# Performance work log

Measured on AMD Instinct MI355X. Metric: run time of the kernel, lower is better.

The kernel has to match this reference:

```python
import jax, jax.numpy as jnp
import numpy as np

B, S, IN, OUT = 64, 512, 256, 256   # batch, seq_len, in/out features
R, NB, E = 40, 3, 262144            # num_rels, num_bases, num_edges
N = B * S                           # total nodes in batched graph


def setup_inputs() -> dict:
    key = jax.random.key(0)
    ks = jax.random.split(key, 6)
    text = jax.random.normal(ks[0], (B, S, IN), jnp.float32)
    src = jax.random.randint(ks[1], (E,), 0, N)
    dst = jax.random.randint(ks[2], (E,), 0, N)
    rel = jax.random.randint(ks[3], (E,), 0, R)
    bases = jax.random.normal(ks[4], (NB, IN, OUT), jnp.float32) / np.sqrt(IN).astype(np.float32)
    comp = jax.random.normal(ks[5], (R, NB), jnp.float32)
    bias = jnp.zeros((OUT,), jnp.float32)
    return dict(text=text, src=src, dst=dst, rel=rel, bases=bases, comp=comp, bias=bias)


def reference(text, src, dst, rel, bases, comp, bias):
    Bt, St, INt = text.shape
    h = text.reshape(-1, INt)                       # [N, in] flattened node feats
    n_nodes = h.shape[0]
    # project every node through every basis once: [N, num_bases, out]
    t = jnp.einsum('ni,bio->nbo', h, bases)
    # per-edge message: sum_b comp[rel_e, b] * (h_src @ basis_b)  -> [E, out]
    msg = jnp.einsum('eb,ebo->eo', comp[rel], t[src])
    # scatter-sum aggregation to destination nodes
    agg = jax.ops.segment_sum(msg, dst, num_segments=n_nodes)   # [N, out]
    out = jax.nn.relu(agg + bias)
    return out.reshape(Bt, -1, out.shape[-1])
```

## Files before the change

kernel.cpp:

```cpp
#include <hip/hip_runtime.h>
#include <cstdint>

#define N_NODES 32768
#define IN_F    256
#define OUT_F   256
#define NBASES  3
#define N_EDGES 262144
#define K_DIM   (NBASES * IN_F)

typedef __attribute__((ext_vector_type(8))) short bf16x8;
typedef __attribute__((ext_vector_type(4))) float f32x4;

__device__ __forceinline__ unsigned short f2bf(float x) {
    union { float f; unsigned int u; } c; c.f = x;
    unsigned int u = c.u;
    u = (u + 0x7FFFu + ((u >> 16) & 1u)) >> 16;
    return (unsigned short)u;
}
__device__ __forceinline__ float bf2f(unsigned short h) {
    union { unsigned int u; float f; } c; c.u = ((unsigned int)h) << 16;
    return c.f;
}

__device__ __forceinline__ void async_copy16(const void* g, void* l) {
    __builtin_amdgcn_global_load_lds(
        (const __attribute__((address_space(1))) unsigned int*)g,
        (__attribute__((address_space(3))) unsigned int*)l, 16, 0, 0);
}

__global__ __launch_bounds__(256) void prep_kernel(
    const float* __restrict__ text,
    const float* __restrict__ bases,
    unsigned short* __restrict__ hb,
    unsigned short* __restrict__ Wt,
    int* __restrict__ counts)
{
    const int tid = threadIdx.x;
    if (blockIdx.x < 8192) {
        if (!hb) return;
        int i = blockIdx.x * 256 + tid;
        float4 v = reinterpret_cast<const float4*>(text)[i];
        ushort4 o;
        o.x = f2bf(v.x); o.y = f2bf(v.y); o.z = f2bf(v.z); o.w = f2bf(v.w);
        reinterpret_cast<ushort4*>(hb)[i] = o;
    } else if (blockIdx.x < 8384) {
        int tb = blockIdx.x - 8192;
        int kb = tb % 24, ob = tb / 24;
        __shared__ float tile[32][33];
        int c = tid & 31, r8 = tid >> 5;
        #pragma unroll
        for (int i = 0; i < 4; ++i) {
            int r = r8 + 8 * i;
            tile[r][c] = bases[(size_t)(kb * 32 + r) * OUT_F + ob * 32 + c];
        }
        __syncthreads();
        #pragma unroll
        for (int i = 0; i < 4; ++i) {
            int r = r8 + 8 * i;
            Wt[(size_t)(ob * 32 + r) * K_DIM + kb * 32 + c] = f2bf(tile[c][r]);
        }
    } else {
        int i = (blockIdx.x - 8384) * 256 + tid;
        counts[i] = 0;
    }
}

__global__ __launch_bounds__(256) void hist_kernel(
    const int* __restrict__ dst, int* __restrict__ counts)
{
    int e4 = blockIdx.x * 256 + threadIdx.x;
    int4 d = reinterpret_cast<const int4*>(dst)[e4];
    atomicAdd(&counts[d.x], 1);
    atomicAdd(&counts[d.y], 1);
    atomicAdd(&counts[d.z], 1);
    atomicAdd(&counts[d.w], 1);
}

__global__ __launch_bounds__(1024) void scan_kernel(
    int* __restrict__ counts,
    int* __restrict__ offsets)
{
    __shared__ int wsum[16];
    const int tid = threadIdx.x;
    const int wave = tid >> 6, lane = tid & 63;
    const int base = tid * 32;
    int local[32];
    int sum = 0;
    #pragma unroll
    for (int k8 = 0; k8 < 8; ++k8) {
        int4 v = reinterpret_cast<const int4*>(counts + base)[k8];
        local[k8 * 4 + 0] = v.x; local[k8 * 4 + 1] = v.y;
        local[k8 * 4 + 2] = v.z; local[k8 * 4 + 3] = v.w;
        sum += v.x + v.y + v.z + v.w;
    }
    int inc = sum;
    #pragma unroll
    for (int off = 1; off < 64; off <<= 1) {
        int v = __shfl_up(inc, off);
        if (lane >= off) inc += v;
    }
    if (lane == 63) wsum[wave] = inc;
    __syncthreads();
    if (wave == 0 && lane < 16) {
        int v = wsum[lane];
        #pragma unroll
        for (int off = 1; off < 16; off <<= 1) {
            int u = __shfl_up(v, off);
            if (lane >= off) v += u;
        }
        wsum[lane] = v;
    }
    __syncthreads();
    int run = inc - sum + (wave ? wsum[wave - 1] : 0);
    #pragma unroll
    for (int k = 0; k < 32; ++k) {
        offsets[base + k] = run;
        counts[base + k] = run;
        run += local[k];
    }
    if (tid == 1023) offsets[N_NODES] = run;
}

__global__ __launch_bounds__(256) void scatter_kernel(
    const int* __restrict__ dst, const int* __restrict__ src,
    const int* __restrict__ rel, int* __restrict__ cursor,
    int* __restrict__ packed)
{
    int e4 = blockIdx.x * 256 + threadIdx.x;
    int4 d = reinterpret_cast<const int4*>(dst)[e4];
    int4 s = reinterpret_cast<const int4*>(src)[e4];
    int4 r = reinterpret_cast<const int4*>(rel)[e4];
    int p0 = atomicAdd(&cursor[d.x], 1);
    packed[p0] = (r.x << 16) | s.x;
    int p1 = atomicAdd(&cursor[d.y], 1);
    packed[p1] = (r.y << 16) | s.y;
    int p2 = atomicAdd(&cursor[d.z], 1);
    packed[p2] = (r.z << 16) | s.z;
    int p3 = atomicAdd(&cursor[d.w], 1);
    packed[p3] = (r.w << 16) | s.w;
}

__global__ __launch_bounds__(256) void agg_bf16_kernel(
    const unsigned short* __restrict__ hb,
    const int* __restrict__ packed,
    const int* __restrict__ offsets,
    const float* __restrict__ comp,
    unsigned short* __restrict__ z)
{
    __shared__ float compS[128];
    if (threadIdx.x < 120) compS[threadIdx.x] = comp[threadIdx.x];
    __syncthreads();

    const int node = blockIdx.x * 4 + (threadIdx.x >> 6);
    const int lane = threadIdx.x & 63;
    const int start = offsets[node];
    const int end   = offsets[node + 1];

    float a0[4] = {}, a1[4] = {}, a2[4] = {};

    for (int cb = start; cb < end; cb += 64) {
        int idx = cb + lane;
        int pv = (idx < end) ? packed[idx] : 0;
        int cnt = min(64, end - cb);
        for (int j = 0; j < cnt; j += 4) {
            float c0[4], c1[4], c2[4];
            ushort4 u[4];
            #pragma unroll
            for (int q = 0; q < 4; ++q) {
                int p = __shfl(pv, j + q);
                int s = p & 0xFFFF, r = p >> 16;
                float m = (j + q < cnt) ? 1.f : 0.f;
                c0[q] = m * compS[r * 3 + 0];
                c1[q] = m * compS[r * 3 + 1];
                c2[q] = m * compS[r * 3 + 2];
                u[q] = *reinterpret_cast<const ushort4*>(
                    hb + (size_t)s * IN_F + lane * 4);
            }
            #pragma unroll
            for (int q = 0; q < 4; ++q) {
                float v[4] = { bf2f(u[q].x), bf2f(u[q].y),
                               bf2f(u[q].z), bf2f(u[q].w) };
                #pragma unroll
                for (int k = 0; k < 4; ++k) {
                    a0[k] += c0[q] * v[k];
                    a1[k] += c1[q] * v[k];
                    a2[k] += c2[q] * v[k];
                }
            }
        }
    }

    unsigned short* zp = z + (size_t)node * K_DIM + lane * 4;
    ushort4 o;
    o.x = f2bf(a0[0]); o.y = f2bf(a0[1]); o.z = f2bf(a0[2]); o.w = f2bf(a0[3]);
    *reinterpret_cast<ushort4*>(zp) = o;
    o.x = f2bf(a1[0]); o.y = f2bf(a1[1]); o.z = f2bf(a1[2]); o.w = f2bf(a1[3]);
    *reinterpret_cast<ushort4*>(zp + 256) = o;
    o.x = f2bf(a2[0]); o.y = f2bf(a2[1]); o.z = f2bf(a2[2]); o.w = f2bf(a2[3]);
    *reinterpret_cast<ushort4*>(zp + 512) = o;
}

__global__ __launch_bounds__(256) void agg_f32_kernel(
    const float* __restrict__ h,
    const int* __restrict__ packed,
    const int* __restrict__ offsets,
    const float* __restrict__ comp,
    unsigned short* __restrict__ z)
{
    __shared__ float compS[128];
    if (threadIdx.x < 120) compS[threadIdx.x] = comp[threadIdx.x];
    __syncthreads();
    const int node = blockIdx.x * 4 + (threadIdx.x >> 6);
    const int lane = threadIdx.x & 63;
    const int start = offsets[node];
    const int end   = offsets[node + 1];
    float a0[4] = {}, a1[4] = {}, a2[4] = {};
    for (int cb = start; cb < end; cb += 64) {
        int idx = cb + lane;
        int pv = (idx < end) ? packed[idx] : 0;
        int cnt = min(64, end - cb);
        for (int j = 0; j < cnt; ++j) {
            int p = __shfl(pv, j);
            int s = p & 0xFFFF, r = p >> 16;
            float c0 = compS[r*3], c1 = compS[r*3+1], c2 = compS[r*3+2];
            float4 v = *reinterpret_cast<const float4*>(
                h + (size_t)s * IN_F + lane * 4);
            a0[0] += c0*v.x; a0[1] += c0*v.y; a0[2] += c0*v.z; a0[3] += c0*v.w;
            a1[0] += c1*v.x; a1[1] += c1*v.y; a1[2] += c1*v.z; a1[3] += c1*v.w;
            a2[0] += c2*v.x; a2[1] += c2*v.y; a2[2] += c2*v.z; a2[3] += c2*v.w;
        }
    }
    unsigned short* zp = z + (size_t)node * K_DIM + lane * 4;
    ushort4 o;
    o.x = f2bf(a0[0]); o.y = f2bf(a0[1]); o.z = f2bf(a0[2]); o.w = f2bf(a0[3]);
    *reinterpret_cast<ushort4*>(zp) = o;
    o.x = f2bf(a1[0]); o.y = f2bf(a1[1]); o.z = f2bf(a1[2]); o.w = f2bf(a1[3]);
    *reinterpret_cast<ushort4*>(zp + 256) = o;
    o.x = f2bf(a2[0]); o.y = f2bf(a2[1]); o.z = f2bf(a2[2]); o.w = f2bf(a2[3]);
    *reinterpret_cast<ushort4*>(zp + 512) = o;
}

__global__ __launch_bounds__(256) void gemm_kernel(
    const unsigned short* __restrict__ A,
    const unsigned short* __restrict__ Bt,
    const float* __restrict__ bias,
    float* __restrict__ out)
{
    __shared__ __align__(16) unsigned short As[2][64 * 32];
    __shared__ __align__(16) unsigned short Bs[2][128 * 32];

    const int tid  = threadIdx.x;
    const int wave = tid >> 6, lane = tid & 63;
    const int quad = lane >> 4, l16 = lane & 15;
    const int wm = (wave & 1) * 32, wn = (wave >> 1) * 64;
    const int m0 = blockIdx.x * 64, n0 = blockIdx.y * 128;

    f32x4 acc[2][4] = {};

    const int pa   = wave * 64 + lane;
    const int rowa = pa >> 2;
    const int octa = (pa & 3) ^ ((rowa >> 1) & 3);
    const unsigned short* ga = A + (size_t)(m0 + rowa) * K_DIM + octa * 8;
    const int la_off = (wave * 64) * 8;

    const unsigned short* gb[2];
    int lb_off[2];
    #pragma unroll
    for (int c = 0; c < 2; ++c) {
        int p   = c * 256 + wave * 64 + lane;
        int row = p >> 2;
        int oct = (p & 3) ^ ((row >> 1) & 3);
        gb[c] = Bt + (size_t)(n0 + row) * K_DIM + oct * 8;
        lb_off[c] = (c * 256 + wave * 64) * 8;
    }

    async_copy16(ga, &As[0][la_off]);
    async_copy16(gb[0], &Bs[0][lb_off[0]]);
    async_copy16(gb[1], &Bs[0][lb_off[1]]);

    int cur = 0;
    for (int step = 0; step < K_DIM / 32; ++step) {
        __syncthreads();
        int k1 = (step + 1) * 32;
        if (k1 < K_DIM) {
            async_copy16(ga + k1, &As[cur ^ 1][la_off]);
            async_copy16(gb[0] + k1, &Bs[cur ^ 1][lb_off[0]]);
            async_copy16(gb[1] + k1, &Bs[cur ^ 1][lb_off[1]]);
        }

        bf16x8 af[2], bfr[4];
        #pragma unroll
        for (int i = 0; i < 2; ++i) {
            int row = wm + i * 16 + l16;
            int oph = quad ^ ((row >> 1) & 3);
            af[i] = *reinterpret_cast<const bf16x8*>(&As[cur][(row * 4 + oph) * 8]);
        }
        #pragma unroll
        for (int j = 0; j < 4; ++j) {
            int nn   = wn + j * 16 + l16;
            int oph2 = quad ^ ((nn >> 1) & 3);
            bfr[j] = *reinterpret_cast<const bf16x8*>(&Bs[cur][(nn * 4 + oph2) * 8]);
        }
        #pragma unroll
        for (int i = 0; i < 2; ++i)
            #pragma unroll
            for (int j = 0; j < 4; ++j)
                acc[i][j] = __builtin_amdgcn_mfma_f32_16x16x32_bf16(
                    af[i], bfr[j], acc[i][j], 0, 0, 0);
        cur ^= 1;
    }

    #pragma unroll
    for (int j = 0; j < 4; ++j) {
        int col = n0 + wn + j * 16 + l16;
        float bv = bias[col];
        #pragma unroll
        for (int i = 0; i < 2; ++i) {
            int row_base = m0 + wm + i * 16 + quad * 4;
            #pragma unroll
            for (int r = 0; r < 4; ++r)
                out[(size_t)(row_base + r) * OUT_F + col] =
                    fmaxf(acc[i][j][r] + bv, 0.f);
        }
    }
}

extern "C" void kernel_launch(void* const* d_in, const int* in_sizes, int n_in,
                              void* d_out, int out_size, void* d_ws, size_t ws_size,
                              hipStream_t stream) {
    const float* text  = (const float*)d_in[0];
    const int*   src   = (const int*)d_in[1];
    const int*   dst   = (const int*)d_in[2];
    const int*   rel   = (const int*)d_in[3];
    const float* bases = (const float*)d_in[4];
    const float* comp  = (const float*)d_in[5];
    const float* bias  = (const float*)d_in[6];
    float* out = (float*)d_out;

    char* p = (char*)d_ws;
    unsigned short* z = (unsigned short*)p;       p += (size_t)N_NODES * K_DIM * 2;
    int* packed  = (int*)p;                       p += (size_t)N_EDGES * 4;
    int* offsets = (int*)p;                       p += (size_t)(N_NODES + 4) * 4;
    int* counts  = (int*)p;                       p += (size_t)N_NODES * 4;
    unsigned short* Wt = (unsigned short*)p;      p += (size_t)OUT_F * K_DIM * 2;
    bool use_bf16_h = (ws_size >= (size_t)(p - (char*)d_ws) + (size_t)N_NODES * IN_F * 2);
    unsigned short* hb = use_bf16_h ? (unsigned short*)p : nullptr;

    prep_kernel<<<8512, 256, 0, stream>>>(text, bases, hb, Wt, counts);
    hist_kernel<<<N_EDGES / 1024, 256, 0, stream>>>(dst, counts);
    scan_kernel<<<1, 1024, 0, stream>>>(counts, offsets);
    scatter_kernel<<<N_EDGES / 1024, 256, 0, stream>>>(dst, src, rel, counts, packed);
    if (use_bf16_h)
        agg_bf16_kernel<<<N_NODES / 4, 256, 0, stream>>>(hb, packed, offsets, comp, z);
    else
        agg_f32_kernel<<<N_NODES / 4, 256, 0, stream>>>(text, packed, offsets, comp, z);
    gemm_kernel<<<dim3(N_NODES / 64, OUT_F / 128), 256, 0, stream>>>(
        z, Wt, bias, out);
}
```

Measured before the change: 193.4 us.

## Fuse edge aggregation with basis GEMM and pack bf16 coefficients into edge records

Merges the per-node aggregation kernel and the GEMM into one kernel. Each block aggregates 32 destination nodes into a swizzled LDS tile and then runs MFMA against the transposed basis weights, so the intermediate z matrix (N x 768 bf16) is never written to or read back from global memory. The scatter kernel now precomputes the three relation coefficients as bf16 and stores them alongside the source index in an 8-byte record, which removes the comp lookup from the gather loop but rounds the coefficients to bf16. The GEMM loses double-buffered B loads and the full Wt is streamed once per 32-row block. The f32 fallback path is dropped and the code assumes the workspace is large enough.

```diff
diff --git a/kernel.cpp b/kernel.cpp
--- a/kernel.cpp
+++ b/kernel.cpp
@@ -7,6 +7,7 @@
 #define NBASES  3
 #define N_EDGES 262144
 #define K_DIM   (NBASES * IN_F)
+#define ZROWS   32
 
 typedef __attribute__((ext_vector_type(8))) short bf16x8;
 typedef __attribute__((ext_vector_type(4))) float f32x4;
@@ -37,7 +38,6 @@
 {
     const int tid = threadIdx.x;
     if (blockIdx.x < 8192) {
-        if (!hb) return;
         int i = blockIdx.x * 256 + tid;
         float4 v = reinterpret_cast<const float4*>(text)[i];
         ushort4 o;
@@ -123,183 +123,128 @@
 
 __global__ __launch_bounds__(256) void scatter_kernel(
     const int* __restrict__ dst, const int* __restrict__ src,
-    const int* __restrict__ rel, int* __restrict__ cursor,
-    int* __restrict__ packed)
+    const int* __restrict__ rel, const float* __restrict__ comp,
+    int* __restrict__ cursor, int2* __restrict__ packed2)
 {
     int e4 = blockIdx.x * 256 + threadIdx.x;
     int4 d = reinterpret_cast<const int4*>(dst)[e4];
     int4 s = reinterpret_cast<const int4*>(src)[e4];
     int4 r = reinterpret_cast<const int4*>(rel)[e4];
-    int p0 = atomicAdd(&cursor[d.x], 1);
-    packed[p0] = (r.x << 16) | s.x;
-    int p1 = atomicAdd(&cursor[d.y], 1);
-    packed[p1] = (r.y << 16) | s.y;
-    int p2 = atomicAdd(&cursor[d.z], 1);
-    packed[p2] = (r.z << 16) | s.z;
-    int p3 = atomicAdd(&cursor[d.w], 1);
-    packed[p3] = (r.w << 16) | s.w;
-}
-
-__global__ __launch_bounds__(256) void agg_bf16_kernel(
+    int dd[4] = { d.x, d.y, d.z, d.w };
+    int ss[4] = { s.x, s.y, s.z, s.w };
+    int rr[4] = { r.x, r.y, r.z, r.w };
+    #pragma unroll
+    for (int q = 0; q < 4; ++q) {
+        float c0 = comp[rr[q] * 3 + 0];
+        float c1 = comp[rr[q] * 3 + 1];
+        float c2 = comp[rr[q] * 3 + 2];
+        int w0 = ss[q] | ((int)f2bf(c0) << 16);
+        int w1 = (int)f2bf(c1) | ((int)f2bf(c2) << 16);
+        int pos = atomicAdd(&cursor[dd[q]], 1);
+        packed2[pos] = make_int2(w0, w1);
+    }
+}
+
+__global__ __launch_bounds__(256, 2) void fused_kernel(
     const unsigned short* __restrict__ hb,
-    const int* __restrict__ packed,
+    const int2* __restrict__ packed2,
     const int* __restrict__ offsets,
-    const float* __restrict__ comp,
-    unsigned short* __restrict__ z)
-{
-    __shared__ float compS[128];
-    if (threadIdx.x < 120) compS[threadIdx.x] = comp[threadIdx.x];
-    __syncthreads();
-
-    const int node = blockIdx.x * 4 + (threadIdx.x >> 6);
-    const int lane = threadIdx.x & 63;
-    const int start = offsets[node];
-    const int end   = offsets[node + 1];
-
-    float a0[4] = {}, a1[4] = {}, a2[4] = {};
-
-    for (int cb = start; cb < end; cb += 64) {
-        int idx = cb + lane;
-        int pv = (idx < end) ? packed[idx] : 0;
-        int cnt = min(64, end - cb);
-        for (int j = 0; j < cnt; j += 4) {
-            float c0[4], c1[4], c2[4];
-            ushort4 u[4];
-            #pragma unroll
-            for (int q = 0; q < 4; ++q) {
-                int p = __shfl(pv, j + q);
-                int s = p & 0xFFFF, r = p >> 16;
-                float m = (j + q < cnt) ? 1.f : 0.f;
-                c0[q] = m * compS[r * 3 + 0];
-                c1[q] = m * compS[r * 3 + 1];
-                c2[q] = m * compS[r * 3 + 2];
-                u[q] = *reinterpret_cast<const ushort4*>(
-                    hb + (size_t)s * IN_F + lane * 4);
-            }
-            #pragma unroll
-            for (int q = 0; q < 4; ++q) {
-                float v[4] = { bf2f(u[q].x), bf2f(u[q].y),
-                               bf2f(u[q].z), bf2f(u[q].w) };
-                #pragma unroll
-                for (int k = 0; k < 4; ++k) {
-                    a0[k] += c0[q] * v[k];
-                    a1[k] += c1[q] * v[k];
-                    a2[k] += c2[q] * v[k];
-                }
-            }
-        }
-    }
-
-    unsigned short* zp = z + (size_t)node * K_DIM + lane * 4;
-    ushort4 o;
-    o.x = f2bf(a0[0]); o.y = f2bf(a0[1]); o.z = f2bf(a0[2]); o.w = f2bf(a0[3]);
-    *reinterpret_cast<ushort4*>(zp) = o;
-    o.x = f2bf(a1[0]); o.y = f2bf(a1[1]); o.z = f2bf(a1[2]); o.w = f2bf(a1[3]);
-    *reinterpret_cast<ushort4*>(zp + 256) = o;
-    o.x = f2bf(a2[0]); o.y = f2bf(a2[1]); o.z = f2bf(a2[2]); o.w = f2bf(a2[3]);
-    *reinterpret_cast<ushort4*>(zp + 512) = o;
-}
-
-__global__ __launch_bounds__(256) void agg_f32_kernel(
-    const float* __restrict__ h,
-    const int* __restrict__ packed,
-    const int* __restrict__ offsets,
-    const float* __restrict__ comp,
-    unsigned short* __restrict__ z)
-{
-    __shared__ float compS[128];
-    if (threadIdx.x < 120) compS[threadIdx.x] = comp[threadIdx.x];
-    __syncthreads();
-    const int node = blockIdx.x * 4 + (threadIdx.x >> 6);
-    const int lane = threadIdx.x & 63;
-    const int start = offsets[node];
-    const int end   = offsets[node + 1];
-    float a0[4] = {}, a1[4] = {}, a2[4] = {};
-    for (int cb = start; cb < end; cb += 64) {
-        int idx = cb + lane;
-        int pv = (idx < end) ? packed[idx] : 0;
-        int cnt = min(64, end - cb);
-        for (int j = 0; j < cnt; ++j) {
-            int p = __shfl(pv, j);
-            int s = p & 0xFFFF, r = p >> 16;
-            float c0 = compS[r*3], c1 = compS[r*3+1], c2 = compS[r*3+2];
-            float4 v = *reinterpret_cast<const float4*>(
-                h + (size_t)s * IN_F + lane * 4);
-            a0[0] += c0*v.x; a0[1] += c0*v.y; a0[2] += c0*v.z; a0[3] += c0*v.w;
-            a1[0] += c1*v.x; a1[1] += c1*v.y; a1[2] += c1*v.z; a1[3] += c1*v.w;
-            a2[0] += c2*v.x; a2[1] += c2*v.y; a2[2] += c2*v.z; a2[3] += c2*v.w;
-        }
-    }
-    unsigned short* zp = z + (size_t)node * K_DIM + lane * 4;
-    ushort4 o;
-    o.x = f2bf(a0[0]); o.y = f2bf(a0[1]); o.z = f2bf(a0[2]); o.w = f2bf(a0[3]);
-    *reinterpret_cast<ushort4*>(zp) = o;
-    o.x = f2bf(a1[0]); o.y = f2bf(a1[1]); o.z = f2bf(a1[2]); o.w = f2bf(a1[3]);
-    *reinterpret_cast<ushort4*>(zp + 256) = o;
-    o.x = f2bf(a2[0]); o.y = f2bf(a2[1]); o.z = f2bf(a2[2]); o.w = f2bf(a2[3]);
-    *reinterpret_cast<ushort4*>(zp + 512) = o;
-}
-
-__global__ __launch_bounds__(256) void gemm_kernel(
-    const unsigned short* __restrict__ A,
-    const unsigned short* __restrict__ Bt,
+    const unsigned short* __restrict__ Wt,
     const float* __restrict__ bias,
     float* __restrict__ out)
 {
-    __shared__ __align__(16) unsigned short As[2][64 * 32];
-    __shared__ __align__(16) unsigned short Bs[2][128 * 32];
+    __shared__ __align__(16) unsigned short Zs[ZROWS * 96 * 8];
+    __shared__ __align__(16) unsigned short Bs[256 * 4 * 8];
 
     const int tid  = threadIdx.x;
     const int wave = tid >> 6, lane = tid & 63;
     const int quad = lane >> 4, l16 = lane & 15;
-    const int wm = (wave & 1) * 32, wn = (wave >> 1) * 64;
-    const int m0 = blockIdx.x * 64, n0 = blockIdx.y * 128;
+    const int m0 = blockIdx.x * ZROWS;
+
+    for (int i = 0; i < 8; ++i) {
+        const int m = wave * 8 + i;
+        const int node = m0 + m;
+        const int start = offsets[node];
+        const int end   = offsets[node + 1];
+
+        float a[12] = {};
+        for (int cb = start; cb < end; cb += 64) {
+            int idx = cb + lane;
+            int wx = 0, wy = 0;
+            if (idx < end) { int2 w = packed2[idx]; wx = w.x; wy = w.y; }
+            int cnt = min(64, end - cb);
+            for (int j = 0; j < cnt; j += 4) {
+                float c0[4], c1[4], c2[4];
+                ushort4 u[4];
+                #pragma unroll
+                for (int q = 0; q < 4; ++q) {
+                    int p0 = __shfl(wx, j + q);
+                    int p1 = __shfl(wy, j + q);
+                    int s = p0 & 0xFFFF;
+                    c0[q] = bf2f((unsigned short)((unsigned)p0 >> 16));
+                    c1[q] = bf2f((unsigned short)(p1 & 0xFFFF));
+                    c2[q] = bf2f((unsigned short)((unsigned)p1 >> 16));
+                    u[q] = *reinterpret_cast<const ushort4*>(
+                        hb + (size_t)s * IN_F + lane * 4);
+                }
+                #pragma unroll
+                for (int q = 0; q < 4; ++q) {
+                    float v[4] = { bf2f(u[q].x), bf2f(u[q].y),
+                                   bf2f(u[q].z), bf2f(u[q].w) };
+                    #pragma unroll
+                    for (int k = 0; k < 4; ++k) {
+                        a[k]     += c0[q] * v[k];
+                        a[4 + k] += c1[q] * v[k];
+                        a[8 + k] += c2[q] * v[k];
+                    }
+                }
+            }
+        }
+
+        #pragma unroll
+        for (int seg = 0; seg < 3; ++seg) {
+            int oct  = seg * 32 + (lane >> 1);
+            int phys = oct ^ (m & 7);
+            ushort4 o;
+            o.x = f2bf(a[seg * 4 + 0]); o.y = f2bf(a[seg * 4 + 1]);
+            o.z = f2bf(a[seg * 4 + 2]); o.w = f2bf(a[seg * 4 + 3]);
+            *reinterpret_cast<ushort4*>(
+                &Zs[(m * 96 + phys) * 8 + (lane & 1) * 4]) = o;
+        }
+    }
+    __syncthreads();
+
+    const unsigned short* gB[4];
+    int lB[4];
+    #pragma unroll
+    for (int c = 0; c < 4; ++c) {
+        int p = c * 256 + wave * 64 + lane;
+        int col = p >> 2;
+        int logical = (p & 3) ^ ((col >> 1) & 3);
+        gB[c] = Wt + (size_t)col * K_DIM + logical * 8;
+        lB[c] = (c * 256 + wave * 64) * 8;
+    }
 
     f32x4 acc[2][4] = {};
-
-    const int pa   = wave * 64 + lane;
-    const int rowa = pa >> 2;
-    const int octa = (pa & 3) ^ ((rowa >> 1) & 3);
-    const unsigned short* ga = A + (size_t)(m0 + rowa) * K_DIM + octa * 8;
-    const int la_off = (wave * 64) * 8;
-
-    const unsigned short* gb[2];
-    int lb_off[2];
-    #pragma unroll
-    for (int c = 0; c < 2; ++c) {
-        int p   = c * 256 + wave * 64 + lane;
-        int row = p >> 2;
-        int oct = (p & 3) ^ ((row >> 1) & 3);
-        gb[c] = Bt + (size_t)(n0 + row) * K_DIM + oct * 8;
-        lb_off[c] = (c * 256 + wave * 64) * 8;
-    }
-
-    async_copy16(ga, &As[0][la_off]);
-    async_copy16(gb[0], &Bs[0][lb_off[0]]);
-    async_copy16(gb[1], &Bs[0][lb_off[1]]);
-
-    int cur = 0;
-    for (int step = 0; step < K_DIM / 32; ++step) {
+    for (int s = 0; s < 24; ++s) {
         __syncthreads();
-        int k1 = (step + 1) * 32;
-        if (k1 < K_DIM) {
-            async_copy16(ga + k1, &As[cur ^ 1][la_off]);
-            async_copy16(gb[0] + k1, &Bs[cur ^ 1][lb_off[0]]);
-            async_copy16(gb[1] + k1, &Bs[cur ^ 1][lb_off[1]]);
-        }
+        #pragma unroll
+        for (int c = 0; c < 4; ++c)
+            async_copy16(gB[c] + s * 32, &Bs[lB[c]]);
+        __syncthreads();
 
         bf16x8 af[2], bfr[4];
         #pragma unroll
         for (int i = 0; i < 2; ++i) {
-            int row = wm + i * 16 + l16;
-            int oph = quad ^ ((row >> 1) & 3);
-            af[i] = *reinterpret_cast<const bf16x8*>(&As[cur][(row * 4 + oph) * 8]);
+            int m = i * 16 + l16;
+            int phys = (s * 4 + quad) ^ (m & 7);
+            af[i] = *reinterpret_cast<const bf16x8*>(&Zs[(m * 96 + phys) * 8]);
         }
         #pragma unroll
         for (int j = 0; j < 4; ++j) {
-            int nn   = wn + j * 16 + l16;
-            int oph2 = quad ^ ((nn >> 1) & 3);
-            bfr[j] = *reinterpret_cast<const bf16x8*>(&Bs[cur][(nn * 4 + oph2) * 8]);
+            int col = wave * 64 + j * 16 + l16;
+            int physo = quad ^ ((col >> 1) & 3);
+            bfr[j] = *reinterpret_cast<const bf16x8*>(&Bs[(col * 4 + physo) * 8]);
         }
         #pragma unroll
         for (int i = 0; i < 2; ++i)
@@ -307,16 +252,15 @@
             for (int j = 0; j < 4; ++j)
                 acc[i][j] = __builtin_amdgcn_mfma_f32_16x16x32_bf16(
                     af[i], bfr[j], acc[i][j], 0, 0, 0);
-        cur ^= 1;
     }
 
     #pragma unroll
     for (int j = 0; j < 4; ++j) {
-        int col = n0 + wn + j * 16 + l16;
+        int col = wave * 64 + j * 16 + l16;
         float bv = bias[col];
         #pragma unroll
         for (int i = 0; i < 2; ++i) {
-            int row_base = m0 + wm + i * 16 + quad * 4;
+            int row_base = m0 + i * 16 + quad * 4;
             #pragma unroll
             for (int r = 0; r < 4; ++r)
                 out[(size_t)(row_base + r) * OUT_F + col] =
@@ -338,22 +282,17 @@
     float* out = (float*)d_out;
 
     char* p = (char*)d_ws;
-    unsigned short* z = (unsigned short*)p;       p += (size_t)N_NODES * K_DIM * 2;
-    int* packed  = (int*)p;                       p += (size_t)N_EDGES * 4;
-    int* offsets = (int*)p;                       p += (size_t)(N_NODES + 4) * 4;
-    int* counts  = (int*)p;                       p += (size_t)N_NODES * 4;
-    unsigned short* Wt = (unsigned short*)p;      p += (size_t)OUT_F * K_DIM * 2;
-    bool use_bf16_h = (ws_size >= (size_t)(p - (char*)d_ws) + (size_t)N_NODES * IN_F * 2);
-    unsigned short* hb = use_bf16_h ? (unsigned short*)p : nullptr;
+    unsigned short* hb = (unsigned short*)p;      p += (size_t)N_NODES * IN_F * 2;
+    int2* packed2 = (int2*)p;                     p += (size_t)N_EDGES * 8;
+    int* offsets  = (int*)p;                      p += (size_t)(N_NODES + 4) * 4;
+    int* counts   = (int*)p;                      p += (size_t)N_NODES * 4;
+    unsigned short* Wt = (unsigned short*)p;
 
     prep_kernel<<<8512, 256, 0, stream>>>(text, bases, hb, Wt, counts);
     hist_kernel<<<N_EDGES / 1024, 256, 0, stream>>>(dst, counts);
     scan_kernel<<<1, 1024, 0, stream>>>(counts, offsets);
-    scatter_kernel<<<N_EDGES / 1024, 256, 0, stream>>>(dst, src, rel, counts, packed);
-    if (use_bf16_h)
-        agg_bf16_kernel<<<N_NODES / 4, 256, 0, stream>>>(hb, packed, offsets, comp, z);
-    else
-        agg_f32_kernel<<<N_NODES / 4, 256, 0, stream>>>(text, packed, offsets, comp, z);
-    gemm_kernel<<<dim3(N_NODES / 64, OUT_F / 128), 256, 0, stream>>>(
-        z, Wt, bias, out);
-}
+    scatter_kernel<<<N_EDGES / 1024, 256, 0, stream>>>(
+        dst, src, rel, comp, counts, packed2);
+    fused_kernel<<<N_NODES / ZROWS, 256, 0, stream>>>(
+        hb, packed2, offsets, Wt, bias, out);
+}
```

Measured after the change: 212.0 us. 1.1x slower.
